# Optimization experiments

Measured on AMD Instinct MI355X. Metric: run time of the kernel, lower is better.

The kernel has to match this reference:

```python
import jax, jax.numpy as jnp
import numpy as np

N = 100_000  # nodes
E = 1_600_000  # edges (avg degree 16)


def _lin_init(key, fan_in, fan_out):
    kw, kb = jax.random.split(key)
    s = 1.0 / np.sqrt(fan_in)
    W = jax.random.uniform(kw, (fan_in, fan_out), minval=-s, maxval=s, dtype=jnp.float32)
    b = jax.random.uniform(kb, (fan_out,), minval=-s, maxval=s, dtype=jnp.float32)
    return W, b


def setup_inputs() -> dict:
    key = jax.random.key(0)
    ks = jax.random.split(key, 14)
    x = jax.random.normal(ks[0], (N, 13), dtype=jnp.float32)
    edge_index = jax.random.randint(ks[1], (2, E), 0, N, dtype=jnp.int32)
    inp = {"x": x, "edge_index": edge_index}
    # lin_query/lin_key/lin_value -> heads*out_channels; lin_skip -> out width
    specs = [("q1", 13, 192), ("k1", 13, 192), ("v1", 13, 192), ("s1", 13, 64),
             ("q2", 64, 192), ("k2", 64, 192), ("v2", 64, 192), ("s2", 64, 64),
             ("q3", 64, 10), ("k3", 64, 10), ("v3", 64, 10), ("s3", 64, 10)]
    for i, (nm, fi, fo) in enumerate(specs):
        W, b = _lin_init(ks[2 + i], fi, fo)
        inp[nm + "_w"] = W
        inp[nm + "_b"] = b
    return inp


def _tconv(x, src, dst, Wq, bq, Wk, bk, Wv, bv, Ws, bs, H, C, concat):
    """PyG TransformerConv (edge_attr=None, beta=False, root_weight=True, dropout off)."""
    q = (x @ Wq + bq).reshape(-1, H, C)[dst]  # [E,H,C] query at target i
    k = (x @ Wk + bk).reshape(-1, H, C)[src]  # [E,H,C] key at source j
    v = (x @ Wv + bv).reshape(-1, H, C)[src]  # [E,H,C] value at source j
    logits = (q * k).sum(-1) * (1.0 / np.sqrt(C))  # [E,H]
    # segment softmax over incoming edges of each target node
    m = jax.ops.segment_max(logits, dst, num_segments=N)
    m = jnp.where(jnp.isfinite(m), m, 0.0)  # empty segments -> -inf -> 0
    e = jnp.exp(logits - m[dst])
    denom = jax.ops.segment_sum(e, dst, num_segments=N)
    alpha = e / (denom[dst] + 1e-16)  # [E,H]
    agg = jax.ops.segment_sum(alpha[:, :, None] * v, dst, num_segments=N)  # [N,H,C]
    out = agg.reshape(-1, H * C) if concat else agg.mean(axis=1)
    return out + x @ Ws + bs  # root/skip connection


def reference(x, edge_index,
              q1_w, q1_b, k1_w, k1_b, v1_w, v1_b, s1_w, s1_b,
              q2_w, q2_b, k2_w, k2_b, v2_w, v2_b, s2_w, s2_b,
              q3_w, q3_b, k3_w, k3_b, v3_w, v3_b, s3_w, s3_b):
    src, dst = edge_index[0], edge_index[1]
    h = jax.nn.relu(_tconv(x, src, dst, q1_w, q1_b, k1_w, k1_b, v1_w, v1_b, s1_w, s1_b, 3, 64, False))
    y = jax.nn.relu(_tconv(h, src, dst, q2_w, q2_b, k2_w, k2_b, v2_w, v2_b, s2_w, s2_b, 3, 64, False))
    h = y + h
    out = _tconv(h, src, dst, q3_w, q3_b, k3_w, k3_b, v3_w, v3_b, s3_w, s3_b, 1, 10, True)
    return jax.nn.log_softmax(out, axis=1)
```

## Files before the change

### kernel.cpp

```cpp
#include <hip/hip_runtime.h>
#include <math.h>

typedef unsigned int u32;
typedef unsigned short u16;


__device__ __forceinline__ float bf2f(u16 u) {
  union { u32 i; float f; } c; c.i = ((u32)u) << 16; return c.f;
}
__device__ __forceinline__ u16 f2bf(float f) {
  union { float f; u32 i; } c; c.f = f;
  u32 u = c.i;
  u32 r = u + 0x7fffu + ((u >> 16) & 1u);
  return (u16)(r >> 16);
}
__device__ __forceinline__ float blo(u32 w) {
  union { u32 i; float f; } c; c.i = w << 16; return c.f;
}
__device__ __forceinline__ float bhi(u32 w) {
  union { u32 i; float f; } c; c.i = w & 0xffff0000u; return c.f;
}

__global__ __launch_bounds__(256) void zero_i32_kernel(int* __restrict__ p, int n) {
  int i = blockIdx.x * blockDim.x + threadIdx.x;
  if (i < n) p[i] = 0;
}

__global__ __launch_bounds__(256) void deg_kernel(
    const int* __restrict__ dst, int* __restrict__ deg, int E) {
  int e = blockIdx.x * blockDim.x + threadIdx.x;
  if (e < E) atomicAdd(&deg[dst[e]], 1);
}

__global__ __launch_bounds__(1024) void scan1_kernel(
    const int* __restrict__ deg, int* __restrict__ excl,
    int* __restrict__ bsum, int n) {
  __shared__ int wsum[16];
  int tid = threadIdx.x;
  int i = blockIdx.x * 1024 + tid;
  int v = (i < n) ? deg[i] : 0;
  int lane = tid & 63, w = tid >> 6;
  int val = v;
#pragma unroll
  for (int off = 1; off < 64; off <<= 1) {
    int t = __shfl_up(val, off, 64);
    if (lane >= off) val += t;
  }
  if (lane == 63) wsum[w] = val;
  __syncthreads();
  if (tid < 16) {
    int xv = wsum[tid];
    int xs = xv;
#pragma unroll
    for (int off = 1; off < 16; off <<= 1) {
      int t = __shfl_up(xs, off, 16);
      if (tid >= off) xs += t;
    }
    wsum[tid] = xs - xv;
  }
  __syncthreads();
  int incl = val + wsum[w];
  if (i < n) excl[i] = incl - v;
  if (tid == 1023) bsum[blockIdx.x] = incl;
}

__global__ __launch_bounds__(1024) void scan2_kernel(int* __restrict__ bsum, int nb) {
  __shared__ int wsum[16];
  int tid = threadIdx.x;
  int v = (tid < nb) ? bsum[tid] : 0;
  int lane = tid & 63, w = tid >> 6;
  int val = v;
#pragma unroll
  for (int off = 1; off < 64; off <<= 1) {
    int t = __shfl_up(val, off, 64);
    if (lane >= off) val += t;
  }
  if (lane == 63) wsum[w] = val;
  __syncthreads();
  if (tid < 16) {
    int xv = wsum[tid];
    int xs = xv;
#pragma unroll
    for (int off = 1; off < 16; off <<= 1) {
      int t = __shfl_up(xs, off, 16);
      if (tid >= off) xs += t;
    }
    wsum[tid] = xs - xv;
  }
  __syncthreads();
  int incl = val + wsum[w];
  if (tid < nb) bsum[tid] = incl - v;
}

__global__ __launch_bounds__(256) void scan3_kernel(
    const int* __restrict__ excl, const int* __restrict__ bsum,
    int* __restrict__ rowptr, int* __restrict__ cursor, int n, int E) {
  int i = blockIdx.x * blockDim.x + threadIdx.x;
  if (i < n) {
    int r = excl[i] + bsum[i >> 10];
    rowptr[i] = r;
    cursor[i] = r;
  }
  if (i == n) rowptr[n] = E;
}

__global__ __launch_bounds__(256) void scatter_kernel(
    const int* __restrict__ src, const int* __restrict__ dst,
    int* __restrict__ cursor, int* __restrict__ csr_src, int E) {
  int e = blockIdx.x * blockDim.x + threadIdx.x;
  if (e < E) {
    int pos = atomicAdd(&cursor[dst[e]], 1);
    csr_src[pos] = src[e];
  }
}

template<int FI, bool XBF>
__global__ __launch_bounds__(256) void kv_proj_v2(
    const void* __restrict__ xin,
    const float* __restrict__ Wk, const float* __restrict__ bk,
    const float* __restrict__ Wv, const float* __restrict__ bv,
    u16* __restrict__ kv, int n_nodes) {
  __shared__ u16 Wlds[FI * 384];
  __shared__ float blds[384];
  int tid = threadIdx.x;
  for (int idx = tid; idx < FI * 384; idx += 256) {
    int i = idx / 384;
    int s = idx - i * 384;
    int g = s / 24;
    int r = s - g * 24;
    int which = r / 12;
    int rr = r - which * 12;
    int h = rr >> 2;
    int cs = rr & 3;
    int o = h * 64 + (g * 4 + cs);
    float w = which ? Wv[i * 192 + o] : Wk[i * 192 + o];
    Wlds[idx] = f2bf(w);
  }
  for (int s = tid; s < 384; s += 256) {
    int g = s / 24;
    int r = s - g * 24;
    int which = r / 12;
    int rr = r - which * 12;
    int h = rr >> 2;
    int cs = rr & 3;
    int o = h * 64 + (g * 4 + cs);
    blds[s] = which ? bv[o] : bk[o];
  }
  __syncthreads();
  int wv = tid >> 6, lane = tid & 63;
  float b0 = blds[lane * 6 + 0], b1 = blds[lane * 6 + 1], b2 = blds[lane * 6 + 2];
  float b3 = blds[lane * 6 + 3], b4 = blds[lane * 6 + 4], b5 = blds[lane * 6 + 5];
#pragma unroll
  for (int t = 0; t < 8; ++t) {
    int n = blockIdx.x * 32 + wv * 8 + t;
    if (n >= n_nodes) break;
    float a0 = b0, a1 = b1, a2 = b2, a3 = b3, a4 = b4, a5 = b5;
    const u16* xb = (const u16*)xin + (size_t)n * FI;
    const float* xf = (const float*)xin + (size_t)n * FI;
#pragma unroll
    for (int i = 0; i < FI; ++i) {
      float xi = XBF ? bf2f(xb[i]) : xf[i];
      const u32* wr = (const u32*)(Wlds + i * 384 + 6 * lane);
      u32 w01 = wr[0], w23 = wr[1], w45 = wr[2];
      a0 = fmaf(xi, blo(w01), a0);
      a1 = fmaf(xi, bhi(w01), a1);
      a2 = fmaf(xi, blo(w23), a2);
      a3 = fmaf(xi, bhi(w23), a3);
      a4 = fmaf(xi, blo(w45), a4);
      a5 = fmaf(xi, bhi(w45), a5);
    }
    u32* outp = (u32*)(kv + (size_t)n * 384) + 3 * lane;
    outp[0] = (u32)f2bf(a0) | ((u32)f2bf(a1) << 16);
    outp[1] = (u32)f2bf(a2) | ((u32)f2bf(a3) << 16);
    outp[2] = (u32)f2bf(a4) | ((u32)f2bf(a5) << 16);
  }
}

template<int FI, bool XBF>
__global__ __launch_bounds__(256) void attn_l12_v3(
    const void* __restrict__ xin,
    const float* __restrict__ Wq, const float* __restrict__ bq,
    const float* __restrict__ Ws, const float* __restrict__ bs,
    const u16* __restrict__ kv,
    const int* __restrict__ rowptr, const int* __restrict__ csr_src,
    const u16* __restrict__ resid,
    u16* __restrict__ hout, int n_nodes) {
  int wid = (blockIdx.x * blockDim.x + threadIdx.x) >> 6;
  int lane = threadIdx.x & 63;
  if (wid >= n_nodes) return;
  float q0 = bq[lane], q1 = bq[64 + lane], q2 = bq[128 + lane];
  float sk = bs[lane];
  {
    const u16* xb = (const u16*)xin + (size_t)wid * FI;
    const float* xf = (const float*)xin + (size_t)wid * FI;
#pragma unroll 4
    for (int i = 0; i < FI; ++i) {
      float xi = XBF ? bf2f(xb[i]) : xf[i];
      q0 = fmaf(xi, Wq[i * 192 + lane], q0);
      q1 = fmaf(xi, Wq[i * 192 + 64 + lane], q1);
      q2 = fmaf(xi, Wq[i * 192 + 128 + lane], q2);
      sk = fmaf(xi, Ws[i * 64 + lane], sk);
    }
  }
  const float scale = 0.125f;
  q0 *= scale; q1 *= scale; q2 *= scale;
  int glane = lane & 15;
  int grp = lane >> 4;
  float qp[3][4], skp[4];
#pragma unroll
  for (int cs = 0; cs < 4; ++cs) {
    int srcl = 4 * glane + cs;
    qp[0][cs] = __shfl(q0, srcl, 64);
    qp[1][cs] = __shfl(q1, srcl, 64);
    qp[2][cs] = __shfl(q2, srcl, 64);
    skp[cs] = __shfl(sk, srcl, 64);
  }
  float m[3] = {-1e30f, -1e30f, -1e30f};
  float sden[3] = {0.f, 0.f, 0.f};
  float acc[3][4] = {{0.f, 0.f, 0.f, 0.f}, {0.f, 0.f, 0.f, 0.f}, {0.f, 0.f, 0.f, 0.f}};
  int beg = rowptr[wid], end = rowptr[wid + 1];
  int el = end - 1;
  for (int base = beg; base < end; base += 8) {
    int e0 = base + grp * 2;
    int e1 = e0 + 1;
    bool v0 = e0 < end, v1 = e1 < end;
    int sa = csr_src[v0 ? e0 : el];
    int sb = csr_src[v1 ? e1 : el];
    const uint4* pa = (const uint4*)(kv + (size_t)sa * 384 + glane * 24);
    const uint4* pb = (const uint4*)(kv + (size_t)sb * 384 + glane * 24);
    uint4 A0 = pa[0], A1 = pa[1], A2 = pa[2];
    uint4 B0 = pb[0], B1 = pb[1], B2 = pb[2];
    float dA[3], dB[3];
#pragma unroll
    for (int h = 0; h < 3; ++h) {
      u32 ka0 = (h == 0) ? A0.x : (h == 1) ? A0.z : A1.x;
      u32 ka1 = (h == 0) ? A0.y : (h == 1) ? A0.w : A1.y;
      u32 kb0 = (h == 0) ? B0.x : (h == 1) ? B0.z : B1.x;
      u32 kb1 = (h == 0) ? B0.y : (h == 1) ? B0.w : B1.y;
      dA[h] = fmaf(qp[h][0], blo(ka0), fmaf(qp[h][1], bhi(ka0),
              fmaf(qp[h][2], blo(ka1), qp[h][3] * bhi(ka1))));
      dB[h] = fmaf(qp[h][0], blo(kb0), fmaf(qp[h][1], bhi(kb0),
              fmaf(qp[h][2], blo(kb1), qp[h][3] * bhi(kb1))));
    }
#pragma unroll
    for (int off = 1; off <= 8; off <<= 1) {
#pragma unroll
      for (int h = 0; h < 3; ++h) {
        dA[h] += __shfl_xor(dA[h], off, 64);
        dB[h] += __shfl_xor(dB[h], off, 64);
      }
    }
#pragma unroll
    for (int h = 0; h < 3; ++h) {
      float pa_ = v0 ? dA[h] : -1e30f;
      float pb_ = v1 ? dB[h] : -1e30f;
      float nm = fmaxf(m[h], fmaxf(pa_, pb_));
      float sc = __expf(m[h] - nm);
      float wa = v0 ? __expf(pa_ - nm) : 0.f;
      float wb = v1 ? __expf(pb_ - nm) : 0.f;
      sden[h] = sden[h] * sc + wa + wb;
      u32 va0 = (h == 0) ? A1.z : (h == 1) ? A2.x : A2.z;
      u32 va1 = (h == 0) ? A1.w : (h == 1) ? A2.y : A2.w;
      u32 vb0 = (h == 0) ? B1.z : (h == 1) ? B2.x : B2.z;
      u32 vb1 = (h == 0) ? B1.w : (h == 1) ? B2.y : B2.w;
      acc[h][0] = fmaf(acc[h][0], sc, fmaf(wa, blo(va0), wb * blo(vb0)));
      acc[h][1] = fmaf(acc[h][1], sc, fmaf(wa, bhi(va0), wb * bhi(vb0)));
      acc[h][2] = fmaf(acc[h][2], sc, fmaf(wa, blo(va1), wb * blo(vb1)));
      acc[h][3] = fmaf(acc[h][3], sc, fmaf(wa, bhi(va1), wb * bhi(vb1)));
      m[h] = nm;
    }
  }
#pragma unroll
  for (int off = 16; off <= 32; off <<= 1) {
#pragma unroll
    for (int h = 0; h < 3; ++h) {
      float mo = __shfl_xor(m[h], off, 64);
      float so = __shfl_xor(sden[h], off, 64);
      float nm = fmaxf(m[h], mo);
      float c1 = __expf(m[h] - nm);
      float c2 = __expf(mo - nm);
      sden[h] = sden[h] * c1 + so * c2;
#pragma unroll
      for (int cs = 0; cs < 4; ++cs) {
        float ao = __shfl_xor(acc[h][cs], off, 64);
        acc[h][cs] = acc[h][cs] * c1 + ao * c2;
      }
      m[h] = nm;
    }
  }
  if (grp == 0) {
    float r0 = 1.f / (sden[0] + 1e-16f);
    float r1 = 1.f / (sden[1] + 1e-16f);
    float r2 = 1.f / (sden[2] + 1e-16f);
    float o_[4];
#pragma unroll
    for (int cs = 0; cs < 4; ++cs) {
      float val = (acc[0][cs] * r0 + acc[1][cs] * r1 + acc[2][cs] * r2) * (1.0f / 3.0f);
      val += skp[cs];
      o_[cs] = fmaxf(val, 0.0f);
    }
    if (resid) {
      uint2 rr = *(const uint2*)(resid + (size_t)wid * 64 + glane * 4);
      o_[0] += blo(rr.x); o_[1] += bhi(rr.x);
      o_[2] += blo(rr.y); o_[3] += bhi(rr.y);
    }
    uint2 pack;
    pack.x = (u32)f2bf(o_[0]) | ((u32)f2bf(o_[1]) << 16);
    pack.y = (u32)f2bf(o_[2]) | ((u32)f2bf(o_[3]) << 16);
    *(uint2*)(hout + (size_t)wid * 64 + glane * 4) = pack;
  }
}

__global__ __launch_bounds__(256) void kv3_proj_kernel(
    const u16* __restrict__ h,
    const float* __restrict__ Wk, const float* __restrict__ bk,
    const float* __restrict__ Wv, const float* __restrict__ bv,
    float* __restrict__ kv3, int n_nodes) {
  int idx = blockIdx.x * blockDim.x + threadIdx.x;
  if (idx >= n_nodes * 20) return;
  int n = idx / 20;
  int r = idx - n * 20;
  int which = r / 10;
  int o = r - which * 10;
  const float* W = which ? Wv : Wk;
  float acc = (which ? bv : bk)[o];
  const u16* hr = h + (size_t)n * 64;
#pragma unroll
  for (int i = 0; i < 64; ++i) acc = fmaf(bf2f(hr[i]), W[i * 10 + o], acc);
  kv3[(size_t)n * 20 + which * 10 + o] = acc;
}

__global__ __launch_bounds__(256) void attn_l3_kernel(
    const u16* __restrict__ h,
    const float* __restrict__ Wq, const float* __restrict__ bq,
    const float* __restrict__ Ws, const float* __restrict__ bs,
    const float* __restrict__ kv3,
    const int* __restrict__ rowptr, const int* __restrict__ csr_src,
    float* __restrict__ out, int n_nodes) {
  int tid = blockIdx.x * blockDim.x + threadIdx.x;
  int wid = tid >> 6;
  int lane = threadIdx.x & 63;
  int grp = lane >> 4;
  int sub = lane & 15;
  int n = wid * 4 + grp;
  bool an = (n < n_nodes);
  bool ca = an && (sub < 10);
  float q = 0.f, sk = 0.f;
  if (ca) { q = bq[sub]; sk = bs[sub]; }
  if (an) {
    const u16* hr = h + (size_t)n * 64;
#pragma unroll 4
    for (int i = 0; i < 64; ++i) {
      float xi = bf2f(hr[i]);
      if (sub < 10) {
        q = fmaf(xi, Wq[i * 10 + sub], q);
        sk = fmaf(xi, Ws[i * 10 + sub], sk);
      }
    }
  }
  q *= 0.31622776601683794f;
  float m = -INFINITY, s = 0.f, a = 0.f;
  int beg = 0, end = 0;
  if (an) { beg = rowptr[n]; end = rowptr[n + 1]; }
  for (int e = beg; e < end; ++e) {
    int srcn = csr_src[e];
    float kk = (sub < 10) ? kv3[(size_t)srcn * 20 + sub] : 0.f;
    float vv = (sub < 10) ? kv3[(size_t)srcn * 20 + 10 + sub] : 0.f;
    float p = q * kk;
    p += __shfl_xor(p, 1, 64);
    p += __shfl_xor(p, 2, 64);
    p += __shfl_xor(p, 4, 64);
    p += __shfl_xor(p, 8, 64);
    float nm = fmaxf(m, p);
    float sc = __expf(m - nm);
    float w = __expf(p - nm);
    s = s * sc + w;
    a = a * sc + w * vv;
    m = nm;
  }
  float z = 0.f;
  if (ca) z = a / (s + 1e-16f) + sk;
  float zm = (sub < 10) ? z : -INFINITY;
  float t;
  t = __shfl_xor(zm, 1, 64); zm = fmaxf(zm, t);
  t = __shfl_xor(zm, 2, 64); zm = fmaxf(zm, t);
  t = __shfl_xor(zm, 4, 64); zm = fmaxf(zm, t);
  t = __shfl_xor(zm, 8, 64); zm = fmaxf(zm, t);
  float ez = (sub < 10) ? __expf(z - zm) : 0.f;
  float se = ez;
  se += __shfl_xor(se, 1, 64);
  se += __shfl_xor(se, 2, 64);
  se += __shfl_xor(se, 4, 64);
  se += __shfl_xor(se, 8, 64);
  float ls = logf(se);
  if (ca) out[(size_t)n * 10 + sub] = (z - zm) - ls;
}

extern "C" void kernel_launch(void* const* d_in, const int* in_sizes, int n_in,
                              void* d_out, int out_size, void* d_ws, size_t ws_size,
                              hipStream_t stream) {
  const float* x = (const float*)d_in[0];
  const int* ei = (const int*)d_in[1];
  const int N = in_sizes[0] / 13;
  const int E = in_sizes[1] / 2;
  const int* esrc = ei;
  const int* edst = ei + E;

  const float* q1w = (const float*)d_in[2];  const float* q1b = (const float*)d_in[3];
  const float* k1w = (const float*)d_in[4];  const float* k1b = (const float*)d_in[5];
  const float* v1w = (const float*)d_in[6];  const float* v1b = (const float*)d_in[7];
  const float* s1w = (const float*)d_in[8];  const float* s1b = (const float*)d_in[9];
  const float* q2w = (const float*)d_in[10]; const float* q2b = (const float*)d_in[11];
  const float* k2w = (const float*)d_in[12]; const float* k2b = (const float*)d_in[13];
  const float* v2w = (const float*)d_in[14]; const float* v2b = (const float*)d_in[15];
  const float* s2w = (const float*)d_in[16]; const float* s2b = (const float*)d_in[17];
  const float* q3w = (const float*)d_in[18]; const float* q3b = (const float*)d_in[19];
  const float* k3w = (const float*)d_in[20]; const float* k3b = (const float*)d_in[21];
  const float* v3w = (const float*)d_in[22]; const float* v3b = (const float*)d_in[23];
  const float* s3w = (const float*)d_in[24]; const float* s3b = (const float*)d_in[25];

  size_t off = 0;
  auto carve = [&](size_t bytes) {
    void* p = (char*)d_ws + off;
    off += (bytes + 255) & ~(size_t)255;
    return p;
  };
  int* deg    = (int*)carve((size_t)N * 4);
  int* excl   = (int*)carve((size_t)N * 4);
  int* bsum   = (int*)carve(4096);
  int* rowptr = (int*)carve((size_t)(N + 1) * 4);
  int* cursor = (int*)carve((size_t)N * 4);
  int* csr    = (int*)carve((size_t)E * 4);
  u16* h1     = (u16*)carve((size_t)N * 64 * 2);
  u16* h2     = (u16*)carve((size_t)N * 64 * 2);
  float* kv3  = (float*)carve((size_t)N * 20 * 4);
  u16* kv     = (u16*)carve((size_t)N * 384 * 2);
  if (off > ws_size) return;

  int nb = (N + 1023) / 1024;
  zero_i32_kernel<<<(N + 255) / 256, 256, 0, stream>>>(deg, N);
  deg_kernel<<<(E + 255) / 256, 256, 0, stream>>>(edst, deg, E);
  scan1_kernel<<<nb, 1024, 0, stream>>>(deg, excl, bsum, N);
  scan2_kernel<<<1, 1024, 0, stream>>>(bsum, nb);
  scan3_kernel<<<(N + 1 + 255) / 256, 256, 0, stream>>>(excl, bsum, rowptr, cursor, N, E);
  scatter_kernel<<<(E + 255) / 256, 256, 0, stream>>>(esrc, edst, cursor, csr, E);

  int attn_blocks = (N + 3) / 4;
  int proj_blocks = (N + 31) / 32;
  kv_proj_v2<13, false><<<proj_blocks, 256, 0, stream>>>(
      x, k1w, k1b, v1w, v1b, kv, N);
  attn_l12_v3<13, false><<<attn_blocks, 256, 0, stream>>>(
      x, q1w, q1b, s1w, s1b, kv, rowptr, csr, nullptr, h1, N);
  kv_proj_v2<64, true><<<proj_blocks, 256, 0, stream>>>(
      h1, k2w, k2b, v2w, v2b, kv, N);
  attn_l12_v3<64, true><<<attn_blocks, 256, 0, stream>>>(
      h1, q2w, q2b, s2w, s2b, kv, rowptr, csr, h1, h2, N);
  kv3_proj_kernel<<<(N * 20 + 255) / 256, 256, 0, stream>>>(
      h2, k3w, k3b, v3w, v3b, kv3, N);
  attn_l3_kernel<<<(N + 15) / 16, 256, 0, stream>>>(
      h2, q3w, q3b, s3w, s3b, kv3, rowptr, csr, (float*)d_out, N);
}
```

Before: 1.299 ms.

## Split query projection into chunked LDS-weight kernel and widen attention edge batch

Query projection moves out of the attention kernel into a separate kernel that stages pre-scaled bf16 weights in LDS, permuted so each lane holds the query components it needs. The projected queries go to a scratch buffer aliased with kv3, processed in 20000-node chunks so they fit. The attention kernel now processes 4 edges per 16-lane group per iteration instead of 2, for more memory-level parallelism on the gathers, and sets a min-blocks launch bound. The cost is extra kernel launches, a bf16 round-trip for q, and higher register pressure.

```diff
diff --git a/kernel.cpp b/kernel.cpp
--- a/kernel.cpp
+++ b/kernel.cpp
@@ -177,18 +177,72 @@
 }
 
 template<int FI, bool XBF>
-__global__ __launch_bounds__(256) void attn_l12_v3(
+__global__ __launch_bounds__(256) void q_proj_kernel(
     const void* __restrict__ xin,
     const float* __restrict__ Wq, const float* __restrict__ bq,
+    u16* __restrict__ qp, int n_start, int n_count) {
+  __shared__ u16 Wlds[FI * 256];
+  __shared__ float blds[192];
+  int tid = threadIdx.x;
+  for (int idx = tid; idx < FI * 256; idx += 256) {
+    int i = idx >> 8;
+    int p = idx & 255;
+    int l = p >> 2, j = p & 3;
+    u16 w = 0;
+    if (j < 3) {
+      int t = 3 * l + j;
+      int g = t / 12, r = t - g * 12;
+      int h = r >> 2, cs = r & 3;
+      int o = h * 64 + 4 * g + cs;
+      w = f2bf(0.125f * Wq[i * 192 + o]);
+    }
+    Wlds[idx] = w;
+  }
+  for (int t = tid; t < 192; t += 256) {
+    int g = t / 12, r = t - g * 12;
+    int h = r >> 2, cs = r & 3;
+    int o = h * 64 + 4 * g + cs;
+    blds[t] = 0.125f * bq[o];
+  }
+  __syncthreads();
+  int wv = tid >> 6, lane = tid & 63;
+  float b0 = blds[3 * lane], b1 = blds[3 * lane + 1], b2 = blds[3 * lane + 2];
+#pragma unroll
+  for (int t = 0; t < 8; ++t) {
+    int nl = blockIdx.x * 32 + wv * 8 + t;
+    if (nl >= n_count) break;
+    int n = n_start + nl;
+    float a0 = b0, a1 = b1, a2 = b2;
+    const u16* xb = (const u16*)xin + (size_t)n * FI;
+    const float* xf = (const float*)xin + (size_t)n * FI;
+#pragma unroll
+    for (int i = 0; i < FI; ++i) {
+      float xi = XBF ? bf2f(xb[i]) : xf[i];
+      const uint2 w = *(const uint2*)(Wlds + i * 256 + 4 * lane);
+      a0 = fmaf(xi, blo(w.x), a0);
+      a1 = fmaf(xi, bhi(w.x), a1);
+      a2 = fmaf(xi, blo(w.y), a2);
+    }
+    u16* o = qp + (size_t)nl * 192 + 3 * lane;
+    o[0] = f2bf(a0); o[1] = f2bf(a1); o[2] = f2bf(a2);
+  }
+}
+
+template<int FI, bool XBF>
+__global__ __launch_bounds__(256, 4) void attn_l12_v4(
+    const void* __restrict__ xin,
+    const u16* __restrict__ qp,
     const float* __restrict__ Ws, const float* __restrict__ bs,
     const u16* __restrict__ kv,
     const int* __restrict__ rowptr, const int* __restrict__ csr_src,
     const u16* __restrict__ resid,
-    u16* __restrict__ hout, int n_nodes) {
-  int wid = (blockIdx.x * blockDim.x + threadIdx.x) >> 6;
+    u16* __restrict__ hout, int n_start, int n_count) {
+  int wl = (blockIdx.x * blockDim.x + threadIdx.x) >> 6;
   int lane = threadIdx.x & 63;
-  if (wid >= n_nodes) return;
-  float q0 = bq[lane], q1 = bq[64 + lane], q2 = bq[128 + lane];
+  if (wl >= n_count) return;
+  int wid = n_start + wl;
+  int glane = lane & 15;
+  int grp = lane >> 4;
   float sk = bs[lane];
   {
     const u16* xb = (const u16*)xin + (size_t)wid * FI;
@@ -196,77 +250,87 @@
 #pragma unroll 4
     for (int i = 0; i < FI; ++i) {
       float xi = XBF ? bf2f(xb[i]) : xf[i];
-      q0 = fmaf(xi, Wq[i * 192 + lane], q0);
-      q1 = fmaf(xi, Wq[i * 192 + 64 + lane], q1);
-      q2 = fmaf(xi, Wq[i * 192 + 128 + lane], q2);
       sk = fmaf(xi, Ws[i * 64 + lane], sk);
     }
   }
-  const float scale = 0.125f;
-  q0 *= scale; q1 *= scale; q2 *= scale;
-  int glane = lane & 15;
-  int grp = lane >> 4;
-  float qp[3][4], skp[4];
-#pragma unroll
-  for (int cs = 0; cs < 4; ++cs) {
-    int srcl = 4 * glane + cs;
-    qp[0][cs] = __shfl(q0, srcl, 64);
-    qp[1][cs] = __shfl(q1, srcl, 64);
-    qp[2][cs] = __shfl(q2, srcl, 64);
-    skp[cs] = __shfl(sk, srcl, 64);
-  }
+  float skp[4];
+#pragma unroll
+  for (int cs = 0; cs < 4; ++cs) skp[cs] = __shfl(sk, 4 * glane + cs, 64);
+  const uint2* qrow = (const uint2*)(qp + (size_t)wl * 192 + glane * 12);
+  uint2 qh0 = qrow[0], qh1 = qrow[1], qh2 = qrow[2];
+  float qpk[3][4];
+  qpk[0][0] = blo(qh0.x); qpk[0][1] = bhi(qh0.x);
+  qpk[0][2] = blo(qh0.y); qpk[0][3] = bhi(qh0.y);
+  qpk[1][0] = blo(qh1.x); qpk[1][1] = bhi(qh1.x);
+  qpk[1][2] = blo(qh1.y); qpk[1][3] = bhi(qh1.y);
+  qpk[2][0] = blo(qh2.x); qpk[2][1] = bhi(qh2.x);
+  qpk[2][2] = blo(qh2.y); qpk[2][3] = bhi(qh2.y);
+
   float m[3] = {-1e30f, -1e30f, -1e30f};
   float sden[3] = {0.f, 0.f, 0.f};
-  float acc[3][4] = {{0.f, 0.f, 0.f, 0.f}, {0.f, 0.f, 0.f, 0.f}, {0.f, 0.f, 0.f, 0.f}};
+  float acc[3][4] = {{0.f,0.f,0.f,0.f},{0.f,0.f,0.f,0.f},{0.f,0.f,0.f,0.f}};
   int beg = rowptr[wid], end = rowptr[wid + 1];
   int el = end - 1;
-  for (int base = beg; base < end; base += 8) {
-    int e0 = base + grp * 2;
-    int e1 = e0 + 1;
-    bool v0 = e0 < end, v1 = e1 < end;
-    int sa = csr_src[v0 ? e0 : el];
-    int sb = csr_src[v1 ? e1 : el];
-    const uint4* pa = (const uint4*)(kv + (size_t)sa * 384 + glane * 24);
-    const uint4* pb = (const uint4*)(kv + (size_t)sb * 384 + glane * 24);
-    uint4 A0 = pa[0], A1 = pa[1], A2 = pa[2];
-    uint4 B0 = pb[0], B1 = pb[1], B2 = pb[2];
-    float dA[3], dB[3];
+  for (int base = beg; base < end; base += 16) {
+    int e0 = base + grp * 4;
+    bool vld[4];
+    int src[4];
+#pragma unroll
+    for (int e = 0; e < 4; ++e) {
+      vld[e] = (e0 + e) < end;
+      src[e] = csr_src[vld[e] ? (e0 + e) : el];
+    }
+    uint4 KV[4][3];
+#pragma unroll
+    for (int e = 0; e < 4; ++e) {
+      const uint4* p = (const uint4*)(kv + (size_t)src[e] * 384 + glane * 24);
+      KV[e][0] = p[0]; KV[e][1] = p[1]; KV[e][2] = p[2];
+    }
+    float d[4][3];
+#pragma unroll
+    for (int e = 0; e < 4; ++e) {
+      d[e][0] = fmaf(qpk[0][0], blo(KV[e][0].x), fmaf(qpk[0][1], bhi(KV[e][0].x),
+                fmaf(qpk[0][2], blo(KV[e][0].y), qpk[0][3] * bhi(KV[e][0].y))));
+      d[e][1] = fmaf(qpk[1][0], blo(KV[e][0].z), fmaf(qpk[1][1], bhi(KV[e][0].z),
+                fmaf(qpk[1][2], blo(KV[e][0].w), qpk[1][3] * bhi(KV[e][0].w))));
+      d[e][2] = fmaf(qpk[2][0], blo(KV[e][1].x), fmaf(qpk[2][1], bhi(KV[e][1].x),
+                fmaf(qpk[2][2], blo(KV[e][1].y), qpk[2][3] * bhi(KV[e][1].y))));
+    }
+#pragma unroll
+    for (int off = 1; off <= 8; off <<= 1) {
+#pragma unroll
+      for (int e = 0; e < 4; ++e) {
+#pragma unroll
+        for (int h = 0; h < 3; ++h) d[e][h] += __shfl_xor(d[e][h], off, 64);
+      }
+    }
 #pragma unroll
     for (int h = 0; h < 3; ++h) {
-      u32 ka0 = (h == 0) ? A0.x : (h == 1) ? A0.z : A1.x;
-      u32 ka1 = (h == 0) ? A0.y : (h == 1) ? A0.w : A1.y;
-      u32 kb0 = (h == 0) ? B0.x : (h == 1) ? B0.z : B1.x;
-      u32 kb1 = (h == 0) ? B0.y : (h == 1) ? B0.w : B1.y;
-      dA[h] = fmaf(qp[h][0], blo(ka0), fmaf(qp[h][1], bhi(ka0),
-              fmaf(qp[h][2], blo(ka1), qp[h][3] * bhi(ka1))));
-      dB[h] = fmaf(qp[h][0], blo(kb0), fmaf(qp[h][1], bhi(kb0),
-              fmaf(qp[h][2], blo(kb1), qp[h][3] * bhi(kb1))));
-    }
-#pragma unroll
-    for (int off = 1; off <= 8; off <<= 1) {
-#pragma unroll
-      for (int h = 0; h < 3; ++h) {
-        dA[h] += __shfl_xor(dA[h], off, 64);
-        dB[h] += __shfl_xor(dB[h], off, 64);
+      float p0 = vld[0] ? d[0][h] : -1e30f;
+      float p1 = vld[1] ? d[1][h] : -1e30f;
+      float p2 = vld[2] ? d[2][h] : -1e30f;
+      float p3 = vld[3] ? d[3][h] : -1e30f;
+      float nm = fmaxf(fmaxf(m[h], fmaxf(p0, p1)), fmaxf(p2, p3));
+      float sc = __expf(m[h] - nm);
+      float w0 = vld[0] ? __expf(p0 - nm) : 0.f;
+      float w1 = vld[1] ? __expf(p1 - nm) : 0.f;
+      float w2 = vld[2] ? __expf(p2 - nm) : 0.f;
+      float w3 = vld[3] ? __expf(p3 - nm) : 0.f;
+      sden[h] = fmaf(sden[h], sc, (w0 + w1) + (w2 + w3));
+      u32 Va[4], Vb[4];
+#pragma unroll
+      for (int e = 0; e < 4; ++e) {
+        Va[e] = (h == 0) ? KV[e][1].z : (h == 1) ? KV[e][2].x : KV[e][2].z;
+        Vb[e] = (h == 0) ? KV[e][1].w : (h == 1) ? KV[e][2].y : KV[e][2].w;
       }
-    }
-#pragma unroll
-    for (int h = 0; h < 3; ++h) {
-      float pa_ = v0 ? dA[h] : -1e30f;
-      float pb_ = v1 ? dB[h] : -1e30f;
-      float nm = fmaxf(m[h], fmaxf(pa_, pb_));
-      float sc = __expf(m[h] - nm);
-      float wa = v0 ? __expf(pa_ - nm) : 0.f;
-      float wb = v1 ? __expf(pb_ - nm) : 0.f;
-      sden[h] = sden[h] * sc + wa + wb;
-      u32 va0 = (h == 0) ? A1.z : (h == 1) ? A2.x : A2.z;
-      u32 va1 = (h == 0) ? A1.w : (h == 1) ? A2.y : A2.w;
-      u32 vb0 = (h == 0) ? B1.z : (h == 1) ? B2.x : B2.z;
-      u32 vb1 = (h == 0) ? B1.w : (h == 1) ? B2.y : B2.w;
-      acc[h][0] = fmaf(acc[h][0], sc, fmaf(wa, blo(va0), wb * blo(vb0)));
-      acc[h][1] = fmaf(acc[h][1], sc, fmaf(wa, bhi(va0), wb * bhi(vb0)));
-      acc[h][2] = fmaf(acc[h][2], sc, fmaf(wa, blo(va1), wb * blo(vb1)));
-      acc[h][3] = fmaf(acc[h][3], sc, fmaf(wa, bhi(va1), wb * bhi(vb1)));
+      acc[h][0] = fmaf(acc[h][0], sc, fmaf(w0, blo(Va[0]), fmaf(w1, blo(Va[1]),
+                   fmaf(w2, blo(Va[2]), w3 * blo(Va[3])))));
+      acc[h][1] = fmaf(acc[h][1], sc, fmaf(w0, bhi(Va[0]), fmaf(w1, bhi(Va[1]),
+                   fmaf(w2, bhi(Va[2]), w3 * bhi(Va[3])))));
+      acc[h][2] = fmaf(acc[h][2], sc, fmaf(w0, blo(Vb[0]), fmaf(w1, blo(Vb[1]),
+                   fmaf(w2, blo(Vb[2]), w3 * blo(Vb[3])))));
+      acc[h][3] = fmaf(acc[h][3], sc, fmaf(w0, bhi(Vb[0]), fmaf(w1, bhi(Vb[1]),
+                   fmaf(w2, bhi(Vb[2]), w3 * bhi(Vb[3])))));
       m[h] = nm;
     }
   }
@@ -425,6 +489,7 @@
     off += (bytes + 255) & ~(size_t)255;
     return p;
   };
+  const int CHUNK = 20000;
   int* deg    = (int*)carve((size_t)N * 4);
   int* excl   = (int*)carve((size_t)N * 4);
   int* bsum   = (int*)carve(4096);
@@ -433,7 +498,9 @@
   int* csr    = (int*)carve((size_t)E * 4);
   u16* h1     = (u16*)carve((size_t)N * 64 * 2);
   u16* h2     = (u16*)carve((size_t)N * 64 * 2);
-  float* kv3  = (float*)carve((size_t)N * 20 * 4);
+  void* shared_region = carve((size_t)N * 20 * 4);
+  float* kv3 = (float*)shared_region;
+  u16* qp    = (u16*)shared_region;
   u16* kv     = (u16*)carve((size_t)N * 384 * 2);
   if (off > ws_size) return;
 
@@ -445,16 +512,25 @@
   scan3_kernel<<<(N + 1 + 255) / 256, 256, 0, stream>>>(excl, bsum, rowptr, cursor, N, E);
   scatter_kernel<<<(E + 255) / 256, 256, 0, stream>>>(esrc, edst, cursor, csr, E);
 
-  int attn_blocks = (N + 3) / 4;
   int proj_blocks = (N + 31) / 32;
   kv_proj_v2<13, false><<<proj_blocks, 256, 0, stream>>>(
       x, k1w, k1b, v1w, v1b, kv, N);
-  attn_l12_v3<13, false><<<attn_blocks, 256, 0, stream>>>(
-      x, q1w, q1b, s1w, s1b, kv, rowptr, csr, nullptr, h1, N);
+  for (int c0 = 0; c0 < N; c0 += CHUNK) {
+    int cn = (N - c0 < CHUNK) ? (N - c0) : CHUNK;
+    q_proj_kernel<13, false><<<(cn + 31) / 32, 256, 0, stream>>>(
+        x, q1w, q1b, qp, c0, cn);
+    attn_l12_v4<13, false><<<(cn + 3) / 4, 256, 0, stream>>>(
+        x, qp, s1w, s1b, kv, rowptr, csr, nullptr, h1, c0, cn);
+  }
   kv_proj_v2<64, true><<<proj_blocks, 256, 0, stream>>>(
       h1, k2w, k2b, v2w, v2b, kv, N);
-  attn_l12_v3<64, true><<<attn_blocks, 256, 0, stream>>>(
-      h1, q2w, q2b, s2w, s2b, kv, rowptr, csr, h1, h2, N);
+  for (int c0 = 0; c0 < N; c0 += CHUNK) {
+    int cn = (N - c0 < CHUNK) ? (N - c0) : CHUNK;
+    q_proj_kernel<64, true><<<(cn + 31) / 32, 256, 0, stream>>>(
+        h1, q2w, q2b, qp, c0, cn);
+    attn_l12_v4<64, true><<<(cn + 3) / 4, 256, 0, stream>>>(
+        h1, qp, s2w, s2b, kv, rowptr, csr, h1, h2, c0, cn);
+  }
   kv3_proj_kernel<<<(N * 20 + 255) / 256, 256, 0, stream>>>(
       h2, k3w, k3b, v3w, v3b, kv3, N);
   attn_l3_kernel<<<(N + 15) / 16, 256, 0, stream>>>(
```

Result: slower. 1.553 ms (+19.6%).
